# Performance work log

Measured on AMD Instinct MI355X. Metric: run time of the kernel, lower is better.

Reference implementation:

```python
import jax, jax.numpy as jnp
import numpy as np

N_NODES = 100_000
N_EDGES = 3_200_000
N_ELEMS = 10

# ase.data.covalent_radii (Cordero 2008), missing = 0.2, padded to 119 entries
_COV = [0.2, 0.31, 0.28, 1.28, 0.96, 0.84, 0.76, 0.71, 0.66, 0.57, 0.58, 1.66,
        1.41, 1.21, 1.11, 1.07, 1.05, 1.02, 1.06, 2.03, 1.76, 1.70, 1.60, 1.53,
        1.39, 1.39, 1.32, 1.26, 1.24, 1.32, 1.22, 1.22, 1.20, 1.19, 1.20, 1.20,
        1.16, 2.20, 1.95, 1.90, 1.75, 1.64, 1.54, 1.47, 1.46, 1.42, 1.39, 1.45,
        1.44, 1.42, 1.39, 1.39, 1.38, 1.39, 1.40, 2.44, 2.15, 2.07, 2.04, 2.03,
        2.01, 1.99, 1.98, 1.98, 1.96, 1.94, 1.92, 1.92, 1.89, 1.90, 1.87, 1.87,
        1.75, 1.70, 1.62, 1.51, 1.44, 1.41, 1.36, 1.36, 1.32, 1.45, 1.46, 1.48,
        1.40, 1.50, 1.50, 2.60, 2.21, 2.15, 2.06, 2.00, 1.96, 1.90, 1.87, 1.80,
        1.69] + [0.2] * 22
COVALENT_RADII = jnp.asarray(np.array(_COV, dtype=np.float32))
C = jnp.asarray(np.array([0.1818, 0.5099, 0.2802, 0.02817], dtype=np.float32))
P = 6.0          # polynomial cutoff order
A_EXP = 0.3
A_PREF = 0.4543


def setup_inputs() -> dict:
    key = jax.random.key(0)
    k1, k2, k3, k4 = jax.random.split(key, 4)
    # per-edge distances in a physically plausible range (strictly > 0)
    x = jax.random.uniform(k1, (N_EDGES, 1), dtype=jnp.float32, minval=0.5, maxval=4.5)
    edge_index = jax.random.randint(k2, (2, N_EDGES), 0, N_NODES)
    # one-hot node element attributes
    elem_idx = jax.random.randint(k3, (N_NODES,), 0, N_ELEMS)
    node_attrs = jax.nn.one_hot(elem_idx, N_ELEMS, dtype=jnp.float32)
    # atomic number per element type, in [1, 90)
    atomic_numbers = jax.random.randint(k4, (N_ELEMS,), 1, 90)
    return {"x": x, "node_attrs": node_attrs, "edge_index": edge_index,
            "atomic_numbers": atomic_numbers}


def _poly_envelope(x, r_max, p):
    r = x / r_max
    env = (1.0 - (p + 1.0) * (p + 2.0) / 2.0 * jnp.power(r, p)
           + p * (p + 2.0) * jnp.power(r, p + 1.0)
           - p * (p + 1.0) / 2.0 * jnp.power(r, p + 2.0))
    return env * (x < r_max)


def reference(x, node_attrs, edge_index, atomic_numbers):
    sender, receiver = edge_index[0], edge_index[1]
    # gather per-node atomic numbers via one-hot argmax, then per-edge
    node_Z = atomic_numbers[jnp.argmax(node_attrs, axis=1)][:, None]  # [N,1]
    Z_u = node_Z[sender].astype(jnp.int32)  # [E,1]
    Z_v = node_Z[receiver].astype(jnp.int32)  # [E,1]
    Zu_f = Z_u.astype(x.dtype)
    Zv_f = Z_v.astype(x.dtype)
    a = A_PREF * 0.529 / (jnp.power(Zu_f, A_EXP) + jnp.power(Zv_f, A_EXP))
    r_over_a = x / a
    phi = (C[0] * jnp.exp(-3.2 * r_over_a) + C[1] * jnp.exp(-0.9423 * r_over_a)
           + C[2] * jnp.exp(-0.4028 * r_over_a) + C[3] * jnp.exp(-0.2016 * r_over_a))
    v_edges = 14.3996 * Zu_f * Zv_f / x * phi  # [E,1]
    r_max = (COVALENT_RADII[Z_u] + COVALENT_RADII[Z_v]).astype(x.dtype)  # [E,1]
    v_edges = 0.5 * v_edges * _poly_envelope(x, r_max, jnp.asarray(P, x.dtype))
    V_ZBL = jax.ops.segment_sum(v_edges, receiver, num_segments=node_attrs.shape[0])
    return jnp.squeeze(V_ZBL, axis=-1)  # [N]
```

## Files before the change

### kernel.cpp

```cpp
#include <hip/hip_runtime.h>

#define NELEMS 10
#define W_SHIFT 10
#define W 1024
#define MAXBL 128
#define CHUNK 4096
#define EPT 8
#define BS 512
#define PAD 4
#define SLABCAP (CHUNK + MAXBL * (PAD - 1))
#define PKCAP 50176
#define GRIDP 512
#define INV_A_PREF (1.0f / (0.4543f * 0.529f))

__constant__ float c_cov[119] = {
    0.2f, 0.31f, 0.28f, 1.28f, 0.96f, 0.84f, 0.76f, 0.71f, 0.66f, 0.57f, 0.58f, 1.66f,
    1.41f, 1.21f, 1.11f, 1.07f, 1.05f, 1.02f, 1.06f, 2.03f, 1.76f, 1.70f, 1.60f, 1.53f,
    1.39f, 1.39f, 1.32f, 1.26f, 1.24f, 1.32f, 1.22f, 1.22f, 1.20f, 1.19f, 1.20f, 1.20f,
    1.16f, 2.20f, 1.95f, 1.90f, 1.75f, 1.64f, 1.54f, 1.47f, 1.46f, 1.42f, 1.39f, 1.45f,
    1.44f, 1.42f, 1.39f, 1.39f, 1.38f, 1.39f, 1.40f, 2.44f, 2.15f, 2.07f, 2.04f, 2.03f,
    2.01f, 1.99f, 1.98f, 1.98f, 1.96f, 1.94f, 1.92f, 1.92f, 1.89f, 1.90f, 1.87f, 1.87f,
    1.75f, 1.70f, 1.62f, 1.51f, 1.44f, 1.41f, 1.36f, 1.36f, 1.32f, 1.45f, 1.46f, 1.48f,
    1.40f, 1.50f, 1.50f, 2.60f, 2.21f, 2.15f, 2.06f, 2.00f, 1.96f, 1.90f, 1.87f, 1.80f,
    1.69f,
    0.2f, 0.2f, 0.2f, 0.2f, 0.2f, 0.2f, 0.2f, 0.2f, 0.2f, 0.2f, 0.2f,
    0.2f, 0.2f, 0.2f, 0.2f, 0.2f, 0.2f, 0.2f, 0.2f, 0.2f, 0.2f, 0.2f
};

__device__ __forceinline__ unsigned int pack_vl(float v, int lr) {
    unsigned int b = __float_as_uint(v);
    b += 0x8000u;
    return (b >> 16) | ((unsigned int)lr << 16);
}
__device__ __forceinline__ float unpack_v(unsigned int p) {
    return __uint_as_float(p << 16);
}

__global__ __launch_bounds__(256)
void zbl_node_elem(const float* __restrict__ node_attrs,
                   const int* __restrict__ atomic_numbers,
                   unsigned char* __restrict__ elem,
                   unsigned char* __restrict__ packed,
                   float4* __restrict__ etab_g, int n_nodes) {
    __shared__ float rows[256 * 11];
    __shared__ unsigned char earr[256];
    int t = threadIdx.x;
    if (blockIdx.x == 0 && t < NELEMS) {
        int Z = atomic_numbers[t];
        float zf = (float)Z;
        etab_g[t] = make_float4(zf, powf(zf, 0.3f), c_cov[Z], 0.0f);
    }
    int n0 = blockIdx.x * 256;
    int nrow = min(256, n_nodes - n0);
    int nflt = nrow * NELEMS;
    const float* src = node_attrs + (size_t)n0 * NELEMS;
    for (int i = t; i < nflt; i += 256) {
        int rr = i / NELEMS, cc = i - rr * NELEMS;
        rows[rr * 11 + cc] = src[i];
    }
    __syncthreads();
    if (t < nrow) {
        const float* a = rows + t * 11;
        int best = 0;
        float bv = a[0];
#pragma unroll
        for (int k = 1; k < NELEMS; ++k) {
            float v = a[k];
            if (v > bv) { bv = v; best = k; }
        }
        earr[t] = (unsigned char)best;
        elem[n0 + t] = (unsigned char)best;
    }
    __syncthreads();
    if (t < 128 && 2 * t < nrow) {
        unsigned char lo = earr[2 * t];
        unsigned char hi = (2 * t + 1 < nrow) ? earr[2 * t + 1] : 0;
        packed[(n0 >> 1) + t] = (unsigned char)(lo | (hi << 4));
    }
}

__device__ __forceinline__ float zbl_edge_value_p(float xv, float A, float B,
                                                  float C) {
    float roa = xv * B;
    float phi = 0.1818f  * __expf(-3.2f    * roa)
              + 0.5099f  * __expf(-0.9423f * roa)
              + 0.2802f  * __expf(-0.4028f * roa)
              + 0.02817f * __expf(-0.2016f * roa);
    float v = A / xv * phi;
    float rr = xv / C;
    float rr2 = rr * rr;
    float rr3 = rr2 * rr;
    float rr6 = rr3 * rr3;
    float rr7 = rr6 * rr;
    float rr8 = rr7 * rr;
    float env = 1.0f - 28.0f * rr6 + 48.0f * rr7 - 21.0f * rr8;
    env = (xv < C) ? env : 0.0f;
    return 0.5f * v * env;
}

#define LOADBURST(c, RV, SV, XV)                                          \
    do {                                                                  \
        int _e0 = (c) * CHUNK;                                            \
        const int4*   _rp = (const int4*)(recv + _e0);                    \
        const int4*   _sp = (const int4*)(send + _e0);                    \
        const float4* _xp = (const float4*)(x + _e0);                     \
        int4 _ra = _rp[2 * t], _rb = _rp[2 * t + 1];                      \
        int4 _sa = _sp[2 * t], _sb = _sp[2 * t + 1];                      \
        float4 _xa = _xp[2 * t], _xb = _xp[2 * t + 1];                    \
        RV[0]=_ra.x; RV[1]=_ra.y; RV[2]=_ra.z; RV[3]=_ra.w;               \
        RV[4]=_rb.x; RV[5]=_rb.y; RV[6]=_rb.z; RV[7]=_rb.w;               \
        SV[0]=_sa.x; SV[1]=_sa.y; SV[2]=_sa.z; SV[3]=_sa.w;               \
        SV[4]=_sb.x; SV[5]=_sb.y; SV[6]=_sb.z; SV[7]=_sb.w;               \
        XV[0]=_xa.x; XV[1]=_xa.y; XV[2]=_xa.z; XV[3]=_xa.w;               \
        XV[4]=_xb.x; XV[5]=_xb.y; XV[6]=_xb.z; XV[7]=_xb.w;               \
    } while (0)

#define SCAN_W0()                                                         \
    do {                                                                  \
        if (t < 64) {                                                     \
            int a = (t < nb)      ? ((cntA[t]      + (PAD-1)) & ~(PAD-1)) : 0; \
            int b = (t + 64 < nb) ? ((cntA[t + 64] + (PAD-1)) & ~(PAD-1)) : 0; \
            int a0 = a, b0 = b;                                           \
            _Pragma("unroll")                                             \
            for (int d = 1; d < 64; d <<= 1) {                            \
                int va = __shfl_up(a, d);                                 \
                int vb = __shfl_up(b, d);                                 \
                if (t >= d) { a += va; b += vb; }                         \
            }                                                             \
            int totA = __shfl(a, 63);                                     \
            b += totA;                                                    \
            lds_off[t + 1]  = a;                                          \
            lds_off[t + 65] = b;                                          \
            curB[t]       = a - a0;                                       \
            curB[t + 64]  = b - b0;                                       \
            cntA[t] = 0; cntA[t + 64] = 0;                                \
            if (t == 0) lds_off[0] = 0;                                   \
        }                                                                 \
    } while (0)

__global__ __launch_bounds__(BS)
void zbl_fused(const float* __restrict__ x,
               const int* __restrict__ ei,
               const unsigned char* __restrict__ packed,
               const float4* __restrict__ etab_g,
               int n_edges, int n_nodes, int nb, int slab, int nchunks,
               unsigned int* __restrict__ pg,
               int* __restrict__ offg ) {
    __shared__ unsigned char pk[PKCAP];
    __shared__ unsigned int  pg_s[SLABCAP];
    __shared__ int   lds_off[MAXBL + 1];
    __shared__ int   curB[MAXBL];
    __shared__ int   cntA[MAXBL];
    __shared__ float ptabA[NELEMS * NELEMS];
    __shared__ float ptabB[NELEMS * NELEMS];
    __shared__ float ptabC[NELEMS * NELEMS];

    int t = threadIdx.x;
    const int* send = ei;
    const int* recv = ei + n_edges;

    int c = blockIdx.x;
    if (c >= nchunks) return;

    {
        const unsigned int* ps = (const unsigned int*)packed;
        unsigned int* pd = (unsigned int*)pk;
        int npk = (n_nodes + 1) >> 1;
        int nw = npk >> 2;
        for (int i = t; i < nw; i += BS) pd[i] = ps[i];
        for (int i = (nw << 2) + t; i < npk; i += BS) pk[i] = packed[i];
    }
    for (int i = t; i < (SLABCAP >> 2); i += BS)
        ((uint4*)pg_s)[i] = make_uint4(0u, 0u, 0u, 0u);
    if (t < MAXBL) cntA[t] = 0;
    if (t < NELEMS * NELEMS) {
        float4 u = etab_g[t / NELEMS];
        float4 v = etab_g[t % NELEMS];
        ptabA[t] = 14.3996f * u.x * v.x;
        ptabB[t] = (u.y + v.y) * INV_A_PREF;
        ptabC[t] = u.z + v.z;
    }

    int rv[EPT], sv[EPT];
    float xv[EPT];
    bool full = (c * CHUNK + CHUNK <= n_edges);
    if (full) LOADBURST(c, rv, sv, xv);
    __syncthreads();

    if (full) {
#pragma unroll
        for (int i = 0; i < EPT; ++i) atomicAdd(&cntA[rv[i] >> W_SHIFT], 1);
    } else {
        for (int e = c * CHUNK + t; e < n_edges; e += BS)
            atomicAdd(&cntA[recv[e] >> W_SHIFT], 1);
    }
    __syncthreads();
    SCAN_W0();
    __syncthreads();

    while (true) {
        int n = c + gridDim.x;
        bool has_next = (n < nchunks);
        bool nfull = has_next && (n * CHUNK + CHUNK <= n_edges);
        int rv2[EPT], sv2[EPT];
        float xv2[EPT];
        if (nfull) LOADBURST(n, rv2, sv2, xv2);

        if (full) {
#pragma unroll
            for (int i = 0; i < EPT; ++i) {
                int s = sv[i], r = rv[i];
                int es = (pk[s >> 1] >> ((s & 1) << 2)) & 15;
                int er = (pk[r >> 1] >> ((r & 1) << 2)) & 15;
                int pi = es * NELEMS + er;
                float v = zbl_edge_value_p(xv[i], ptabA[pi], ptabB[pi], ptabC[pi]);
                int pos = atomicAdd(&curB[r >> W_SHIFT], 1);
                pg_s[pos] = pack_vl(v, r & (W - 1));
            }
        } else {
            for (int e = c * CHUNK + t; e < n_edges; e += BS) {
                int s = send[e], r = recv[e];
                int es = (pk[s >> 1] >> ((s & 1) << 2)) & 15;
                int er = (pk[r >> 1] >> ((r & 1) << 2)) & 15;
                int pi = es * NELEMS + er;
                float v = zbl_edge_value_p(x[e], ptabA[pi], ptabB[pi], ptabC[pi]);
                int pos = atomicAdd(&curB[r >> W_SHIFT], 1);
                pg_s[pos] = pack_vl(v, r & (W - 1));
            }
        }
        __syncthreads();

        {
            int total = lds_off[nb];
            uint4* pdst = (uint4*)(pg + (size_t)c * slab);
            int nt4 = total >> 2;
            for (int i = t; i < nt4; i += BS)
                pdst[i] = ((uint4*)pg_s)[i];
            if (t <= nb) offg[c * (nb + 1) + t] = lds_off[t];
        }
        if (has_next) {
            if (nfull) {
#pragma unroll
                for (int i = 0; i < EPT; ++i)
                    atomicAdd(&cntA[rv2[i] >> W_SHIFT], 1);
            } else {
                for (int e = n * CHUNK + t; e < n_edges; e += BS)
                    atomicAdd(&cntA[recv[e] >> W_SHIFT], 1);
            }
        }
        __syncthreads();

        if (!has_next) break;

        if (t >= 64) {
            for (int i = t - 64; i < (SLABCAP >> 2); i += BS - 64)
                ((uint4*)pg_s)[i] = make_uint4(0u, 0u, 0u, 0u);
        } else {
            SCAN_W0();
        }
        __syncthreads();

        c = n;
        full = nfull;
#pragma unroll
        for (int i = 0; i < EPT; ++i) {
            rv[i] = rv2[i]; sv[i] = sv2[i]; xv[i] = xv2[i];
        }
    }
}

__global__ __launch_bounds__(BS)
void zbl_reduce_seg(const unsigned int* __restrict__ pg,
                    const int* __restrict__ offg,
                    int nblk, int nb, int kred, int slab,
                    float* __restrict__ partial) {
    __shared__ float acc[W];
    int b = blockIdx.x;
    int j = blockIdx.y;
    int t = threadIdx.x;
    acc[t] = 0.0f;
    acc[t + BS] = 0.0f;
    __syncthreads();

    int stride = (nblk + kred - 1) / kred;
    int blk0 = j * stride;
    int blk1 = min(nblk, blk0 + stride);
    int wave = t >> 6, lane = t & 63;
    int sw = lane >> 4, li = lane & 15;
    const int NSW = (BS / 64) * 4;

    for (int blk = blk0 + wave * 4 + sw; blk < blk1; blk += NSW) {
        const int* po = offg + (size_t)blk * (nb + 1) + b;
        int s0 = po[0], s1 = po[1];
        const uint4* p4 = (const uint4*)(pg + (size_t)blk * slab);
        for (int q = (s0 >> 2) + li; q < (s1 >> 2); q += 16) {
            uint4 u = p4[q];
            atomicAdd(&acc[u.x >> 16], unpack_v(u.x));
            atomicAdd(&acc[u.y >> 16], unpack_v(u.y));
            atomicAdd(&acc[u.z >> 16], unpack_v(u.z));
            atomicAdd(&acc[u.w >> 16], unpack_v(u.w));
        }
    }
    __syncthreads();
    float* dst = partial + (((size_t)b * kred + j) << W_SHIFT);
    dst[t] = acc[t];
    dst[t + BS] = acc[t + BS];
}

__global__ void zbl_combine(const float* __restrict__ partial, int kred,
                            int n_nodes, float* __restrict__ out) {
    int q = blockIdx.x * blockDim.x + threadIdx.x;
    int n = q << 2;
    if (n >= n_nodes) return;
    int b = n >> W_SHIFT;
    int t = n & (W - 1);
    float4 s = make_float4(0.f, 0.f, 0.f, 0.f);
    for (int j = 0; j < kred; ++j) {
        const float4* p =
            (const float4*)(partial + (((size_t)b * kred + j) << W_SHIFT) + t);
        float4 v = *p;
        s.x += v.x; s.y += v.y; s.z += v.z; s.w += v.w;
    }
    if (n + 3 < n_nodes) {
        *(float4*)(out + n) = s;
    } else {
        out[n] = s.x;
        if (n + 1 < n_nodes) out[n + 1] = s.y;
        if (n + 2 < n_nodes) out[n + 2] = s.z;
    }
}

__global__ void zbl_edge_atomic(const float* __restrict__ x,
                                const int* __restrict__ edge_index,
                                const unsigned char* __restrict__ elem,
                                const float4* __restrict__ etab_g,
                                float* __restrict__ out, int n_edges) {
    int e = blockIdx.x * blockDim.x + threadIdx.x;
    if (e >= n_edges) return;
    int s = edge_index[e];
    int r = edge_index[n_edges + e];
    float4 u = etab_g[elem[s]];
    float4 w = etab_g[elem[r]];
    float v = zbl_edge_value_p(x[e], 14.3996f * u.x * w.x,
                               (u.y + w.y) * INV_A_PREF, u.z + w.z);
#if defined(__HIP_PLATFORM_AMD__)
    unsafeAtomicAdd(out + r, v);
#else
    atomicAdd(out + r, v);
#endif
}

extern "C" void kernel_launch(void* const* d_in, const int* in_sizes, int n_in,
                              void* d_out, int out_size, void* d_ws, size_t ws_size,
                              hipStream_t stream) {
    const float* x              = (const float*)d_in[0];
    const float* node_attrs     = (const float*)d_in[1];
    const int*   edge_index     = (const int*)d_in[2];
    const int*   atomic_numbers = (const int*)d_in[3];
    float*       out            = (float*)d_out;

    int n_edges = in_sizes[0];
    int n_nodes = in_sizes[1] / NELEMS;
    int nb = (n_nodes + W - 1) / W;
    int nblk = (n_edges + CHUNK - 1) / CHUNK;
    int slab = (CHUNK + nb * (PAD - 1) + 3) & ~3;

    char* ws = (char*)d_ws;

    int kred = 0;
    size_t elem_o = 0, pk_o = 0, etab_o = 0,
           pg_o = 0, offg_o = 0, part_o = 0;
    for (int try_k = 8; try_k >= 1; try_k >>= 1) {
        size_t off = 0;
        auto alloc = [&](size_t bytes) {
            size_t o = off;
            off = (off + bytes + 255) & ~(size_t)255;
            return o;
        };
        elem_o = alloc((size_t)n_nodes);
        pk_o   = alloc((size_t)(n_nodes + 1) / 2);
        etab_o = alloc(NELEMS * sizeof(float4));
        pg_o   = alloc((size_t)nblk * slab * sizeof(unsigned int));
        offg_o = alloc((size_t)nblk * (nb + 1) * sizeof(int));
        part_o = alloc((size_t)nb * try_k * W * sizeof(float));
        if (off <= ws_size) { kred = try_k; break; }
    }

    unsigned char* elem   = (unsigned char*)(ws + elem_o);
    unsigned char* packed = (unsigned char*)(ws + pk_o);
    float4* etab_g        = (float4*)(ws + etab_o);

    int nb_nodes = (n_nodes + 255) / 256;
    zbl_node_elem<<<nb_nodes, 256, 0, stream>>>(node_attrs, atomic_numbers,
                                                elem, packed, etab_g, n_nodes);

    bool fast_ok = (kred >= 1) && (nb <= MAXBL) && (slab <= SLABCAP) &&
                   (((n_nodes + 1) >> 1) <= PKCAP);

    if (fast_ok) {
        unsigned int* pg = (unsigned int*)(ws + pg_o);
        int* offg        = (int*)(ws + offg_o);
        float* partial   = (float*)(ws + part_o);

        int gridP = nblk < GRIDP ? nblk : GRIDP;
        zbl_fused<<<gridP, BS, 0, stream>>>(x, edge_index, packed, etab_g,
                                            n_edges, n_nodes, nb, slab, nblk,
                                            pg, offg);
        zbl_reduce_seg<<<dim3(nb, kred), BS, 0, stream>>>(pg, offg, nblk,
                                                          nb, kred, slab, partial);
        int nq = (n_nodes + 3) >> 2;
        zbl_combine<<<(nq + 255) / 256, 256, 0, stream>>>(partial, kred,
                                                          n_nodes, out);
    } else {
        hipMemsetAsync(d_out, 0, (size_t)out_size * sizeof(float), stream);
        int nb_edges = (n_edges + 255) / 256;
        zbl_edge_atomic<<<nb_edges, 256, 0, stream>>>(x, edge_index, elem, etab_g,
                                                      out, n_edges);
    }
}
```

Before: 56.96 us.

## Drop padded per-bucket slabs, handle unaligned bucket edges in reducer, raise kred

Removes the 4-entry padding of each bucket segment in the per-chunk slab, so the LDS slab no longer needs zeroing each iteration and the global slab shrinks to CHUNK entries. The reducer now handles unaligned head and tail elements of each segment with scalar loads and reads the aligned middle with uint4 loads. The partial-sum layout is changed to j-major, and kred may go up to 16 for more reduction parallelism. In exchange, the reducer carries extra scalar edge handling per segment, and the combine kernel has more partials to sum.

Result: no change. 57.07 us, median of 2 (+0.2%).

```diff
diff --git a/kernel.cpp b/kernel.cpp
--- a/kernel.cpp
+++ b/kernel.cpp
@@ -7,8 +7,6 @@
 #define CHUNK 4096
 #define EPT 8
 #define BS 512
-#define PAD 4
-#define SLABCAP (CHUNK + MAXBL * (PAD - 1))
 #define PKCAP 50176
 #define GRIDP 512
 #define INV_A_PREF (1.0f / (0.4543f * 0.529f))
@@ -118,8 +116,8 @@
 #define SCAN_W0()                                                         \
     do {                                                                  \
         if (t < 64) {                                                     \
-            int a = (t < nb)      ? ((cntA[t]      + (PAD-1)) & ~(PAD-1)) : 0; \
-            int b = (t + 64 < nb) ? ((cntA[t + 64] + (PAD-1)) & ~(PAD-1)) : 0; \
+            int a = (t < nb)      ? cntA[t]      : 0;                     \
+            int b = (t + 64 < nb) ? cntA[t + 64] : 0;                     \
             int a0 = a, b0 = b;                                           \
             _Pragma("unroll")                                             \
             for (int d = 1; d < 64; d <<= 1) {                            \
@@ -143,11 +141,11 @@
                const int* __restrict__ ei,
                const unsigned char* __restrict__ packed,
                const float4* __restrict__ etab_g,
-               int n_edges, int n_nodes, int nb, int slab, int nchunks,
+               int n_edges, int n_nodes, int nb, int nchunks,
                unsigned int* __restrict__ pg,
                int* __restrict__ offg ) {
     __shared__ unsigned char pk[PKCAP];
-    __shared__ unsigned int  pg_s[SLABCAP];
+    __shared__ unsigned int  pg_s[CHUNK];
     __shared__ int   lds_off[MAXBL + 1];
     __shared__ int   curB[MAXBL];
     __shared__ int   cntA[MAXBL];
@@ -170,8 +168,6 @@
         for (int i = t; i < nw; i += BS) pd[i] = ps[i];
         for (int i = (nw << 2) + t; i < npk; i += BS) pk[i] = packed[i];
     }
-    for (int i = t; i < (SLABCAP >> 2); i += BS)
-        ((uint4*)pg_s)[i] = make_uint4(0u, 0u, 0u, 0u);
     if (t < MAXBL) cntA[t] = 0;
     if (t < NELEMS * NELEMS) {
         float4 u = etab_g[t / NELEMS];
@@ -232,10 +228,11 @@
 
         {
             int total = lds_off[nb];
-            uint4* pdst = (uint4*)(pg + (size_t)c * slab);
+            unsigned int* gdst = pg + (size_t)c * CHUNK;
             int nt4 = total >> 2;
-            for (int i = t; i < nt4; i += BS)
-                pdst[i] = ((uint4*)pg_s)[i];
+            uint4* p4 = (uint4*)gdst;
+            for (int i = t; i < nt4; i += BS) p4[i] = ((uint4*)pg_s)[i];
+            for (int i = (nt4 << 2) + t; i < total; i += BS) gdst[i] = pg_s[i];
             if (t <= nb) offg[c * (nb + 1) + t] = lds_off[t];
         }
         if (has_next) {
@@ -252,12 +249,7 @@
 
         if (!has_next) break;
 
-        if (t >= 64) {
-            for (int i = t - 64; i < (SLABCAP >> 2); i += BS - 64)
-                ((uint4*)pg_s)[i] = make_uint4(0u, 0u, 0u, 0u);
-        } else {
-            SCAN_W0();
-        }
+        SCAN_W0();
         __syncthreads();
 
         c = n;
@@ -272,7 +264,7 @@
 __global__ __launch_bounds__(BS)
 void zbl_reduce_seg(const unsigned int* __restrict__ pg,
                     const int* __restrict__ offg,
-                    int nblk, int nb, int kred, int slab,
+                    int nblk, int nb, int kred,
                     float* __restrict__ partial) {
     __shared__ float acc[W];
     int b = blockIdx.x;
@@ -287,13 +279,23 @@
     int blk1 = min(nblk, blk0 + stride);
     int wave = t >> 6, lane = t & 63;
     int sw = lane >> 4, li = lane & 15;
-    const int NSW = (BS / 64) * 4;
-
-    for (int blk = blk0 + wave * 4 + sw; blk < blk1; blk += NSW) {
+
+    for (int blk = blk0 + wave * 4 + sw; blk < blk1; blk += 32) {
         const int* po = offg + (size_t)blk * (nb + 1) + b;
         int s0 = po[0], s1 = po[1];
-        const uint4* p4 = (const uint4*)(pg + (size_t)blk * slab);
-        for (int q = (s0 >> 2) + li; q < (s1 >> 2); q += 16) {
+        const unsigned int* base = pg + (size_t)blk * CHUNK;
+        int a0 = (s0 + 3) & ~3; if (a0 > s1) a0 = s1;
+        int a1 = s1 & ~3;       if (a1 < a0) a1 = a0;
+        if (li < a0 - s0) {
+            unsigned int u = base[s0 + li];
+            atomicAdd(&acc[u >> 16], unpack_v(u));
+        }
+        if (li < s1 - a1) {
+            unsigned int u = base[a1 + li];
+            atomicAdd(&acc[u >> 16], unpack_v(u));
+        }
+        const uint4* p4 = (const uint4*)base;
+        for (int q = (a0 >> 2) + li; q < (a1 >> 2); q += 16) {
             uint4 u = p4[q];
             atomicAdd(&acc[u.x >> 16], unpack_v(u.x));
             atomicAdd(&acc[u.y >> 16], unpack_v(u.y));
@@ -302,13 +304,13 @@
         }
     }
     __syncthreads();
-    float* dst = partial + (((size_t)b * kred + j) << W_SHIFT);
+    float* dst = partial + (((size_t)j * nb + b) << W_SHIFT);
     dst[t] = acc[t];
     dst[t + BS] = acc[t + BS];
 }
 
-__global__ void zbl_combine(const float* __restrict__ partial, int kred,
-                            int n_nodes, float* __restrict__ out) {
+__global__ void zbl_combine(const float* __restrict__ partial, int nb,
+                            int kred, int n_nodes, float* __restrict__ out) {
     int q = blockIdx.x * blockDim.x + threadIdx.x;
     int n = q << 2;
     if (n >= n_nodes) return;
@@ -316,8 +318,8 @@
     int t = n & (W - 1);
     float4 s = make_float4(0.f, 0.f, 0.f, 0.f);
     for (int j = 0; j < kred; ++j) {
-        const float4* p =
-            (const float4*)(partial + (((size_t)b * kred + j) << W_SHIFT) + t);
+        const float4* p = (const float4*)(partial +
+            (((size_t)j * nb + b) << W_SHIFT) + t);
         float4 v = *p;
         s.x += v.x; s.y += v.y; s.z += v.z; s.w += v.w;
     }
@@ -363,14 +365,13 @@
     int n_nodes = in_sizes[1] / NELEMS;
     int nb = (n_nodes + W - 1) / W;
     int nblk = (n_edges + CHUNK - 1) / CHUNK;
-    int slab = (CHUNK + nb * (PAD - 1) + 3) & ~3;
 
     char* ws = (char*)d_ws;
 
     int kred = 0;
     size_t elem_o = 0, pk_o = 0, etab_o = 0,
            pg_o = 0, offg_o = 0, part_o = 0;
-    for (int try_k = 8; try_k >= 1; try_k >>= 1) {
+    for (int try_k = 16; try_k >= 1; try_k >>= 1) {
         size_t off = 0;
         auto alloc = [&](size_t bytes) {
             size_t o = off;
@@ -380,7 +381,7 @@
         elem_o = alloc((size_t)n_nodes);
         pk_o   = alloc((size_t)(n_nodes + 1) / 2);
         etab_o = alloc(NELEMS * sizeof(float4));
-        pg_o   = alloc((size_t)nblk * slab * sizeof(unsigned int));
+        pg_o   = alloc((size_t)nblk * CHUNK * sizeof(unsigned int));
         offg_o = alloc((size_t)nblk * (nb + 1) * sizeof(int));
         part_o = alloc((size_t)nb * try_k * W * sizeof(float));
         if (off <= ws_size) { kred = try_k; break; }
@@ -394,7 +395,7 @@
     zbl_node_elem<<<nb_nodes, 256, 0, stream>>>(node_attrs, atomic_numbers,
                                                 elem, packed, etab_g, n_nodes);
 
-    bool fast_ok = (kred >= 1) && (nb <= MAXBL) && (slab <= SLABCAP) &&
+    bool fast_ok = (kred >= 1) && (nb <= MAXBL) &&
                    (((n_nodes + 1) >> 1) <= PKCAP);
 
     if (fast_ok) {
@@ -404,12 +405,12 @@
 
         int gridP = nblk < GRIDP ? nblk : GRIDP;
         zbl_fused<<<gridP, BS, 0, stream>>>(x, edge_index, packed, etab_g,
-                                            n_edges, n_nodes, nb, slab, nblk,
+                                            n_edges, n_nodes, nb, nblk,
                                             pg, offg);
         zbl_reduce_seg<<<dim3(nb, kred), BS, 0, stream>>>(pg, offg, nblk,
-                                                          nb, kred, slab, partial);
+                                                          nb, kred, partial);
         int nq = (n_nodes + 3) >> 2;
-        zbl_combine<<<(nq + 255) / 256, 256, 0, stream>>>(partial, kred,
+        zbl_combine<<<(nq + 255) / 256, 256, 0, stream>>>(partial, nb, kred,
                                                           n_nodes, out);
     } else {
         hipMemsetAsync(d_out, 0, (size_t)out_size * sizeof(float), stream);
```
